# Kernel tuning notes

Hardware: AMD Instinct MI355X
Metric: run time of the kernel (lower is better)

## Reference

```python
import jax, jax.numpy as jnp
import numpy as np

K = 16          # nodes_num
BN_EPS = 1e-5


def _bn_conv_relu(x, w, gamma, beta, mean, var):
    # 1x1 conv on [N,K,C] node features == matmul, then eval-mode BN + ReLU
    y = jnp.einsum('nkc,oc->nko', x, w)                      # [N,K,256]
    y = (y - mean) * jax.lax.rsqrt(var + BN_EPS) * gamma + beta
    return jax.nn.relu(y)


def _lnorm(r, c):
    # Symmetric-normalized affinity from node pixel coordinates.
    # A_ij = 1/(1+||p_i-p_j||), self-loops A_ii=1, Lnorm = D^-1/2 A D^-1/2
    p = jnp.stack([r, c], axis=-1).astype(jnp.float32)        # [N,K,2]
    diff = p[:, :, None, :] - p[:, None, :, :]
    dist = jnp.sqrt(jnp.sum(diff * diff, axis=-1))            # [N,K,K]
    A = 1.0 / (1.0 + dist)
    dinv = jax.lax.rsqrt(jnp.sum(A, axis=-1))                 # [N,K]
    return A * dinv[:, :, None] * dinv[:, None, :]


def setup_inputs() -> dict:
    key = jax.random.key(0)
    ks = jax.random.split(key, 12)
    N, C, W, H = 128, 1024, 14, 14
    O = 256
    inp = {
        'fpam_output': jax.random.normal(ks[0], (N, C, W, H), jnp.float32),
        'resnet_output': jax.random.normal(ks[1], (N, 2048), jnp.float32),
        'w_max': jax.random.normal(ks[2], (O, C), jnp.float32) * 0.02,
        'g_max': 1.0 + 0.1 * jax.random.normal(ks[3], (O,), jnp.float32),
        'b_max': 0.1 * jax.random.normal(ks[4], (O,), jnp.float32),
        'm_max': 0.1 * jax.random.normal(ks[5], (O,), jnp.float32),
        'v_max': jax.random.uniform(ks[6], (O,), jnp.float32, 0.5, 1.5),
        'w_med': jax.random.normal(ks[7], (O, C), jnp.float32) * 0.02,
        'g_med': 1.0 + 0.1 * jax.random.normal(ks[8], (O,), jnp.float32),
        'b_med': 0.1 * jax.random.normal(ks[9], (O,), jnp.float32),
        'm_med': 0.1 * jax.random.normal(ks[10], (O,), jnp.float32),
        'v_med': jax.random.uniform(ks[11], (O,), jnp.float32, 0.5, 1.5),
    }
    return inp


def reference(fpam_output, resnet_output, w_max, g_max, b_max, m_max, v_max,
              w_med, g_med, b_med, m_med, v_med):
    N, C, W, H = fpam_output.shape
    HW = W * H
    # channel-sum saliency, sort descending
    fre = jnp.sum(fpam_output, axis=1).reshape(N, HW)         # [N,HW]
    idx = jnp.argsort(-fre, axis=1)
    maxK = idx[:, :K]
    mstart = HW // 2 - K // 2 - 1
    medK = idx[:, mstart:mstart + K]
    scene = jnp.concatenate([maxK, medK], axis=1)             # [N,2K]
    rows = scene // H
    cols = scene % H
    # batched gather replacing the per-pixel python loop
    flat = fpam_output.reshape(N, C, HW)
    nodes = jnp.take_along_axis(flat, scene[:, None, :], axis=2)  # [N,C,2K]
    nodes = jnp.transpose(nodes, (0, 2, 1))                   # [N,2K,C]
    x_max = _bn_conv_relu(nodes[:, :K], w_max, g_max, b_max, m_max, v_max)
    x_med = _bn_conv_relu(nodes[:, K:], w_med, g_med, b_med, m_med, v_med)
    Ltop = _lnorm(rows[:, :K], cols[:, :K])
    Lmed = _lnorm(rows[:, K:], cols[:, K:])
    max_graph = jnp.einsum('nij,njc->nic', Ltop, x_max).reshape(N, -1)
    med_graph = jnp.einsum('nij,njc->nic', Lmed, x_med).reshape(N, -1)
    return (max_graph, med_graph, rows, cols)
```

## Files before the change

kernel.cpp:

```cpp
#include <hip/hip_runtime.h>

#define NB 128
#define CC 1024
#define HWP 196
#define HH 14
#define OO 256

typedef unsigned short ushort_t;
typedef __attribute__((ext_vector_type(8))) short short8;
typedef __attribute__((ext_vector_type(4))) float float4v;

__device__ __forceinline__ ushort_t f2bf(float v) {
  union { float f; unsigned int u; } c; c.f = v;
  unsigned int u = c.u;
  unsigned int r = (u + 0x7FFFu + ((u >> 16) & 1u)) >> 16;
  return (ushort_t)r;
}

__global__ __launch_bounds__(256) void k_prep(const float* __restrict__ x,
                                              const float* __restrict__ wmax,
                                              const float* __restrict__ wmed,
                                              float* __restrict__ partial,
                                              ushort_t* __restrict__ wb) {
  const int b = blockIdx.x, t = threadIdx.x;
  if (b >= 256) {
    int idx = (b - 256) * 256 + t;
    int z = idx >> 18;
    int r = idx & (OO * CC - 1);
    const float* w = z ? wmed : wmax;
    wb[idx] = f2bf(w[r]);
    return;
  }
  const int unit = b * 4 + (t >> 6);
  const int lane = t & 63;
  if (lane >= 49) return;
  const int n = unit >> 3, cg = unit & 7;
  const float4 * base = (const float4*)(x + ((size_t)n * CC + (size_t)cg * 128) * HWP);
  float4 s = {0.f, 0.f, 0.f, 0.f};
  #pragma unroll 16
  for (int c = 0; c < 128; ++c) {
    float4 v = base[c * 49 + lane];
    s.x += v.x; s.y += v.y; s.z += v.z; s.w += v.w;
  }
  ((float4*)(partial + ((size_t)n * 8 + cg) * HWP))[lane] = s;
}

__global__ __launch_bounds__(256) void k_extract(const float* __restrict__ x,
                                                 const float* __restrict__ partial,
                                                 ushort_t* __restrict__ af) {
  __shared__ float fre[HWP];
  __shared__ int sc[32];

  const int b = blockIdx.x;
  const int n = b >> 2, cg = b & 3;
  const int t = threadIdx.x;

  if (t < HWP) {
    float s = 0.f;
    #pragma unroll
    for (int g = 0; g < 8; ++g) s += partial[((size_t)n * 8 + g) * HWP + t];
    fre[t] = s;
  }
  __syncthreads();
  if (t < HWP) {
    float v = fre[t];
    int rank = 0;
    #pragma unroll 4
    for (int q = 0; q < HWP; ++q) {
      float u = fre[q];
      rank += ((u > v) || (u == v && q < t)) ? 1 : 0;
    }
    if (rank < 16) sc[rank] = t;
    else if (rank >= 89 && rank < 105) sc[rank - 73] = t;
  }
  __syncthreads();

  const int c = cg * 256 + t;
  const float* row = x + ((size_t)n * CC + c) * HWP;
  int sj[32];
  #pragma unroll
  for (int j = 0; j < 32; ++j) sj[j] = sc[j];
  float v[32];
  #pragma unroll
  for (int j = 0; j < 32; ++j) v[j] = row[sj[j]];
  ushort_t* dst = af + (size_t)n * 32 * CC + c;
  #pragma unroll
  for (int j = 0; j < 32; ++j) dst[(size_t)j * CC] = f2bf(v[j]);
}

__global__ __launch_bounds__(512, 2) void k_main(
    const float* __restrict__ partial,
    const ushort_t* __restrict__ wb,
    const ushort_t* __restrict__ af,
    const float* __restrict__ g_max, const float* __restrict__ b_max,
    const float* __restrict__ m_max, const float* __restrict__ v_max,
    const float* __restrict__ g_med, const float* __restrict__ b_med,
    const float* __restrict__ m_med, const float* __restrict__ v_med,
    float* __restrict__ out) {
  constexpr int AP = 1032;
  __shared__ alignas(16) ushort_t A_sh[16 * AP];
  __shared__ float fre[HWP];
  __shared__ int sc[32];
  __shared__ float Lsh[16][17];
  __shared__ float dinv[16];
  __shared__ float y_sh[16][257];

  const int n = blockIdx.x;
  const int z = blockIdx.y;
  const int t = threadIdx.x;

  if (t < HWP) {
    float s = 0.f;
    #pragma unroll
    for (int g = 0; g < 8; ++g) s += partial[((size_t)n * 8 + g) * HWP + t];
    fre[t] = s;
  }
  __syncthreads();
  if (t < HWP) {
    float v = fre[t];
    int rank = 0;
    #pragma unroll 4
    for (int q = 0; q < HWP; ++q) {
      float u = fre[q];
      rank += ((u > v) || (u == v && q < t)) ? 1 : 0;
    }
    if (rank < 16) sc[rank] = t;
    else if (rank >= 89 && rank < 105) sc[rank - 73] = t;
  }
  __syncthreads();

  if (z == 0 && t < 32) {
    int p = sc[t];
    out[2 * NB * 4096 + n * 32 + t] = (float)(p / HH);
    out[2 * NB * 4096 + NB * 32 + n * 32 + t] = (float)(p % HH);
  }

  {
    const int j = t >> 5;
    const int u = t & 31;
    const ushort_t* src = af + ((size_t)n * 32 + z * 16 + j) * CC + u * 8;
    ushort_t* dst = &A_sh[j * AP + u * 8];
    #pragma unroll
    for (int q = 0; q < 4; ++q)
      *(short8*)(dst + q * 256) = *(const short8*)(src + q * 256);
  }
  if (t < 256) {
    const int i = t >> 4, j = t & 15;
    int pi = sc[z * 16 + i], pj = sc[z * 16 + j];
    float dr = (float)(pi / HH - pj / HH);
    float dc = (float)(pi % HH - pj % HH);
    Lsh[i][j] = 1.0f / (1.0f + sqrtf(dr * dr + dc * dc));
  }
  __syncthreads();
  if (t < 16) {
    float s = 0.f;
    #pragma unroll
    for (int j = 0; j < 16; ++j) s += Lsh[t][j];
    dinv[t] = rsqrtf(s);
  }

  const int w = t >> 6;
  const int l = t & 63;
  const int m = l & 15;
  const int quad = l >> 4;

  const ushort_t* Arow = &A_sh[m * AP + quad * 8];
  const ushort_t* B0 = wb + (size_t)z * (OO * CC) + (size_t)(w * 32 + m) * CC + quad * 8;

  float4v acc0 = {0.f, 0.f, 0.f, 0.f};
  float4v acc1 = acc0;

  __syncthreads();

  #pragma unroll 4
  for (int k0 = 0; k0 < CC; k0 += 32) {
    short8 a  = *reinterpret_cast<const short8*>(Arow + k0);
    short8 b0 = *reinterpret_cast<const short8*>(B0 + k0);
    short8 b1 = *reinterpret_cast<const short8*>(B0 + 16 * CC + k0);
    acc0 = __builtin_amdgcn_mfma_f32_16x16x32_bf16(a, b0, acc0, 0, 0, 0);
    acc1 = __builtin_amdgcn_mfma_f32_16x16x32_bf16(a, b1, acc1, 0, 0, 0);
  }

  const float* gp = z ? g_med : g_max;
  const float* bp = z ? b_med : b_max;
  const float* mp = z ? m_med : m_max;
  const float* vp = z ? v_med : v_max;

  #pragma unroll
  for (int tt = 0; tt < 2; ++tt) {
    float4v av = tt ? acc1 : acc0;
    int o = w * 32 + tt * 16 + m;
    float scale = gp[o] * rsqrtf(vp[o] + 1e-5f);
    float shift = bp[o] - mp[o] * scale;
    #pragma unroll
    for (int r = 0; r < 4; ++r) {
      int j = quad * 4 + r;
      float y = av[r] * scale + shift;
      y = fmaxf(y, 0.f);
      y_sh[j][o] = y * dinv[j];
    }
  }
  __syncthreads();

  {
    const int o = t & 255;
    const int ih = (t >> 8) * 8;
    float yp[16];
    #pragma unroll
    for (int j = 0; j < 16; ++j) yp[j] = y_sh[j][o];
    float* ob = out + (size_t)z * (NB * 4096) + (size_t)n * 4096 + o;
    #pragma unroll
    for (int i2 = 0; i2 < 8; ++i2) {
      const int i = ih + i2;
      float s = 0.f;
      #pragma unroll
      for (int j = 0; j < 16; ++j) s = fmaf(Lsh[i][j], yp[j], s);
      ob[(size_t)i * OO] = s * dinv[i];
    }
  }
}

extern "C" void kernel_launch(void* const* d_in, const int* in_sizes, int n_in,
                              void* d_out, int out_size, void* d_ws, size_t ws_size,
                              hipStream_t stream) {
  const float* x     = (const float*)d_in[0];
  const float* w_max = (const float*)d_in[2];
  const float* g_max = (const float*)d_in[3];
  const float* b_max = (const float*)d_in[4];
  const float* m_max = (const float*)d_in[5];
  const float* v_max = (const float*)d_in[6];
  const float* w_med = (const float*)d_in[7];
  const float* g_med = (const float*)d_in[8];
  const float* b_med = (const float*)d_in[9];
  const float* m_med = (const float*)d_in[10];
  const float* v_med = (const float*)d_in[11];
  float* out = (float*)d_out;

  float* ws_f = (float*)d_ws;
  float* partial  = ws_f;
  ushort_t* wb    = (ushort_t*)(ws_f + 200704);
  ushort_t* af    = wb + 2 * OO * CC;

  k_prep<<<dim3(256 + 2048), 256, 0, stream>>>(x, w_max, w_med, partial, wb);
  k_extract<<<dim3(NB * 4), 256, 0, stream>>>(x, partial, af);
  k_main<<<dim3(NB, 2), 512, 0, stream>>>(partial, wb, af,
                                          g_max, b_max, m_max, v_max,
                                          g_med, b_med, m_med, v_med, out);
}
```

Baseline: 237.6 us.

## Stage bf16 copy of input during reduction and gather from it with coalesced writes

The channel-sum prep kernel now also writes a bf16 copy of the full feature map. The node-extraction kernel gathers from this half-size copy instead of the fp32 input. It transposes the gathered values through shared memory so the output rows are written as coalesced 16-byte stores. The goal is to shrink the scattered gather traffic and fix the strided stores, at the cost of an extra large write of the bf16 copy in the prep pass.

New measurement: 269.9 us. 13.6% more time.

```diff
diff --git a/kernel.cpp b/kernel.cpp
--- a/kernel.cpp
+++ b/kernel.cpp
@@ -7,6 +7,7 @@
 #define OO 256
 
 typedef unsigned short ushort_t;
+typedef __attribute__((ext_vector_type(4))) short short4v;
 typedef __attribute__((ext_vector_type(8))) short short8;
 typedef __attribute__((ext_vector_type(4))) float float4v;
 
@@ -21,7 +22,8 @@
                                               const float* __restrict__ wmax,
                                               const float* __restrict__ wmed,
                                               float* __restrict__ partial,
-                                              ushort_t* __restrict__ wb) {
+                                              ushort_t* __restrict__ wb,
+                                              ushort_t* __restrict__ xb16) {
   const int b = blockIdx.x, t = threadIdx.x;
   if (b >= 256) {
     int idx = (b - 256) * 256 + t;
@@ -36,23 +38,29 @@
   if (lane >= 49) return;
   const int n = unit >> 3, cg = unit & 7;
   const float4 * base = (const float4*)(x + ((size_t)n * CC + (size_t)cg * 128) * HWP);
+  ushort_t* xo = xb16 + ((size_t)n * CC + (size_t)cg * 128) * HWP + lane * 4;
   float4 s = {0.f, 0.f, 0.f, 0.f};
   #pragma unroll 16
   for (int c = 0; c < 128; ++c) {
     float4 v = base[c * 49 + lane];
     s.x += v.x; s.y += v.y; s.z += v.z; s.w += v.w;
+    short4v o;
+    o[0] = (short)f2bf(v.x); o[1] = (short)f2bf(v.y);
+    o[2] = (short)f2bf(v.z); o[3] = (short)f2bf(v.w);
+    *(short4v*)(xo + (size_t)c * HWP) = o;
   }
   ((float4*)(partial + ((size_t)n * 8 + cg) * HWP))[lane] = s;
 }
 
-__global__ __launch_bounds__(256) void k_extract(const float* __restrict__ x,
+__global__ __launch_bounds__(256) void k_extract(const ushort_t* __restrict__ xb16,
                                                  const float* __restrict__ partial,
                                                  ushort_t* __restrict__ af) {
   __shared__ float fre[HWP];
   __shared__ int sc[32];
+  __shared__ ushort_t ob[32][264];
 
   const int b = blockIdx.x;
-  const int n = b >> 2, cg = b & 3;
+  const int n = b >> 2, q = b & 3;
   const int t = threadIdx.x;
 
   if (t < HWP) {
@@ -66,26 +74,34 @@
     float v = fre[t];
     int rank = 0;
     #pragma unroll 4
-    for (int q = 0; q < HWP; ++q) {
-      float u = fre[q];
-      rank += ((u > v) || (u == v && q < t)) ? 1 : 0;
+    for (int q2 = 0; q2 < HWP; ++q2) {
+      float u = fre[q2];
+      rank += ((u > v) || (u == v && q2 < t)) ? 1 : 0;
     }
     if (rank < 16) sc[rank] = t;
     else if (rank >= 89 && rank < 105) sc[rank - 73] = t;
   }
   __syncthreads();
 
-  const int c = cg * 256 + t;
-  const float* row = x + ((size_t)n * CC + c) * HWP;
-  int sj[32];
+  {
+    const int j = t & 31, g = t >> 5;
+    const int sp = sc[j];
+    const ushort_t* src = xb16 + ((size_t)n * CC + q * 256 + g * 32) * HWP + sp;
+    ushort_t v[32];
+    #pragma unroll
+    for (int u = 0; u < 32; ++u) v[u] = src[(size_t)u * HWP];
+    #pragma unroll
+    for (int u = 0; u < 32; ++u) ob[j][g * 32 + u] = v[u];
+  }
+  __syncthreads();
+
   #pragma unroll
-  for (int j = 0; j < 32; ++j) sj[j] = sc[j];
-  float v[32];
-  #pragma unroll
-  for (int j = 0; j < 32; ++j) v[j] = row[sj[j]];
-  ushort_t* dst = af + (size_t)n * 32 * CC + c;
-  #pragma unroll
-  for (int j = 0; j < 32; ++j) dst[(size_t)j * CC] = f2bf(v[j]);
+  for (int it = 0; it < 4; ++it) {
+    int f = it * 2048 + t * 8;
+    int jj = f >> 8, cc = f & 255;
+    *(short8*)(af + ((size_t)n * 32 + jj) * CC + q * 256 + cc) =
+        *(const short8*)&ob[jj][cc];
+  }
 }
 
 __global__ __launch_bounds__(512, 2) void k_main(
@@ -208,14 +224,14 @@
     float yp[16];
     #pragma unroll
     for (int j = 0; j < 16; ++j) yp[j] = y_sh[j][o];
-    float* ob = out + (size_t)z * (NB * 4096) + (size_t)n * 4096 + o;
+    float* ob2 = out + (size_t)z * (NB * 4096) + (size_t)n * 4096 + o;
     #pragma unroll
     for (int i2 = 0; i2 < 8; ++i2) {
       const int i = ih + i2;
       float s = 0.f;
       #pragma unroll
       for (int j = 0; j < 16; ++j) s = fmaf(Lsh[i][j], yp[j], s);
-      ob[(size_t)i * OO] = s * dinv[i];
+      ob2[(size_t)i * OO] = s * dinv[i];
     }
   }
 }
@@ -240,9 +256,10 @@
   float* partial  = ws_f;
   ushort_t* wb    = (ushort_t*)(ws_f + 200704);
   ushort_t* af    = wb + 2 * OO * CC;
-
-  k_prep<<<dim3(256 + 2048), 256, 0, stream>>>(x, w_max, w_med, partial, wb);
-  k_extract<<<dim3(NB * 4), 256, 0, stream>>>(x, partial, af);
+  ushort_t* xb16  = af + (size_t)NB * 32 * CC;
+
+  k_prep<<<dim3(256 + 2048), 256, 0, stream>>>(x, w_max, w_med, partial, wb, xb16);
+  k_extract<<<dim3(NB * 4), 256, 0, stream>>>(xb16, partial, af);
   k_main<<<dim3(NB, 2), 512, 0, stream>>>(partial, wb, af,
                                           g_max, b_max, m_max, v_max,
                                           g_med, b_med, m_med, v_med, out);
```
